# Performance work log

Hardware: AMD Instinct MI355X
Metric: run time of the kernel (lower is better)

## Reference

```python
import jax, jax.numpy as jnp
import numpy as np

B, N, D = 2, 4096, 512   # batch, tokens (64x64 latent), query_dim
H, DH = 8, 64            # heads, dim_head; inner_dim = H*DH = 512


def setup_inputs() -> dict:
    key = jax.random.key(0)
    ks = jax.random.split(key, 6)
    s = lambda fan_in: 1.0 / np.sqrt(fan_in)
    x = jax.random.normal(ks[0], (B, N, D), dtype=jnp.float32)
    Wq = jax.random.uniform(ks[1], (D, H * DH), jnp.float32, -s(D), s(D))
    Wk = jax.random.uniform(ks[2], (D, H * DH), jnp.float32, -s(D), s(D))
    Wv = jax.random.uniform(ks[3], (D, H * DH), jnp.float32, -s(D), s(D))
    Wo = jax.random.uniform(ks[4], (H * DH, D), jnp.float32, -s(H * DH), s(H * DH))
    bo = jax.random.uniform(ks[5], (D,), jnp.float32, -s(H * DH), s(H * DH))
    return {"x": x, "Wq": Wq, "Wk": Wk, "Wv": Wv, "Wo": Wo, "bo": bo}


def reference(x, Wq, Wk, Wv, Wo, bo):
    # Self-attention (context = x). Projections (no bias).
    q = x @ Wq  # [B, N, H*DH]
    k = x @ Wk
    v = x @ Wv
    split = lambda t: t.reshape(B, N, H, DH).transpose(0, 2, 1, 3)  # [B, H, N, DH]
    q, k, v = split(q), split(k), split(v)
    scale = DH ** -0.5
    # fp32 upcast for scores (ATTN_PRECISION == 'fp32' path)
    sim = jnp.einsum('bhid,bhjd->bhij', q.astype(jnp.float32), k.astype(jnp.float32)) * scale
    attn = jax.nn.softmax(sim, axis=-1).astype(v.dtype)
    out = jnp.einsum('bhij,bhjd->bhid', attn, v)           # [B, H, N, DH]
    out = out.transpose(0, 2, 1, 3).reshape(B, N, H * DH)  # [B, N, H*DH]
    return out @ Wo + bo  # to_out Linear (dropout=0)
```

## Files before the change

### kernel.cpp

```cpp
#include <hip/hip_runtime.h>
#include <hip/hip_bf16.h>
#include <stdint.h>


typedef short short8 __attribute__((ext_vector_type(8)));
typedef float f32x4 __attribute__((ext_vector_type(4)));
typedef float f32x16 __attribute__((ext_vector_type(16)));

#define QK_SCALE 0.18033688011112042f

static __device__ __forceinline__ unsigned short f32_to_bf16(float f) {
    union { float f; uint32_t u; } v; v.f = f;
    uint32_t u = v.u;
    u += 0x7FFFu + ((u >> 16) & 1u);
    return (unsigned short)(u >> 16);
}

static __device__ __forceinline__ uint32_t cvt_pk_bf16(float lo, float hi) {
    uint32_t r;
    asm("v_cvt_pk_bf16_f32 %0, %1, %2" : "=v"(r) : "v"(lo), "v"(hi));
    return r;
}

static __device__ __forceinline__ int swz(int row, int byte_in_row) {
    return row * 128 + (byte_in_row ^ ((row & 7) << 4));
}

static __device__ __forceinline__ void gload16(const void* g, void* l) {
    __builtin_amdgcn_global_load_lds(
        (const __attribute__((address_space(1))) unsigned int*)g,
        (__attribute__((address_space(3))) unsigned int*)l, 16, 0, 0);
}

union PAU { uint32_t d[4]; short8 v; };

__global__ __launch_bounds__(256) void convert_weights(
    const float* __restrict__ Wq, const float* __restrict__ Wk,
    const float* __restrict__ Wv, const float* __restrict__ Wo,
    unsigned short* __restrict__ wt)
{
    __shared__ float lds[64][65];
    const int mat = blockIdx.z;
    const float* W = (mat == 0) ? Wq : (mat == 1) ? Wk : (mat == 2) ? Wv : Wo;
    const float scale = (mat == 0) ? QK_SCALE : 1.0f;
    unsigned short* out = wt + (size_t)mat * 512 * 512;
    const int k0 = blockIdx.y * 64, n0 = blockIdx.x * 64;
    for (int i = 0; i < 16; i++) {
        int idx = threadIdx.x + i * 256;
        int kl = idx >> 6, nl = idx & 63;
        lds[kl][nl] = W[(size_t)(k0 + kl) * 512 + n0 + nl];
    }
    __syncthreads();
    for (int i = 0; i < 16; i++) {
        int idx = threadIdx.x + i * 256;
        int nr = idx >> 6, kc = idx & 63;
        out[(size_t)(n0 + nr) * 512 + k0 + kc] = f32_to_bf16(lds[kc][nr] * scale);
    }
}

__global__ __launch_bounds__(256) void convert_x(
    const float* __restrict__ x, unsigned short* __restrict__ xbf)
{
    const int idx = (blockIdx.x * 256 + threadIdx.x) * 8;
    float4 f0 = *reinterpret_cast<const float4*>(x + idx);
    float4 f1 = *reinterpret_cast<const float4*>(x + idx + 4);
    short8 v;
    v[0] = (short)f32_to_bf16(f0.x); v[1] = (short)f32_to_bf16(f0.y);
    v[2] = (short)f32_to_bf16(f0.z); v[3] = (short)f32_to_bf16(f0.w);
    v[4] = (short)f32_to_bf16(f1.x); v[5] = (short)f32_to_bf16(f1.y);
    v[6] = (short)f32_to_bf16(f1.z); v[7] = (short)f32_to_bf16(f1.w);
    *reinterpret_cast<short8*>(xbf + idx) = v;
}

__global__ __launch_bounds__(256, 2) void proj_gemm(
    const unsigned short* __restrict__ xbf,
    const unsigned short* __restrict__ wt,
    unsigned short* __restrict__ q_ws,
    unsigned short* __restrict__ k_ws,
    unsigned short* __restrict__ vt_ws)
{
    __shared__ __attribute__((aligned(16))) char smem[65536];
    const int which = blockIdx.z;
    const unsigned short* W = wt + (size_t)which * 512 * 512;
    const int m0 = blockIdx.y * 128, n0 = blockIdx.x * 128;
    const int tid = threadIdx.x, lane = tid & 63, wid = tid >> 6;
    const int wm = (wid >> 1) * 64, wn = (wid & 1) * 64;
    const int rsub = lane >> 3;
    const int cb = ((lane & 7) ^ rsub) << 4;

    f32x4 acc[4][4];
#pragma unroll
    for (int i = 0; i < 4; i++)
#pragma unroll
        for (int j = 0; j < 4; j++) acc[i][j] = (f32x4){0.f, 0.f, 0.f, 0.f};

#define PSTAGE(KT, BUF)                                                           \
    {                                                                             \
        const int kk0_ = (KT) * 64;                                               \
        _Pragma("unroll")                                                         \
        for (int cj = 0; cj < 4; cj++) {                                          \
            const int chunk = wid * 4 + cj;                                       \
            const int row = chunk * 8 + rsub;                                     \
            gload16((const char*)xbf + ((size_t)(m0 + row) * 512 + kk0_) * 2 + cb,\
                    smem + (BUF) * 32768 + chunk * 1024);                         \
            gload16((const char*)W + ((size_t)(n0 + row) * 512 + kk0_) * 2 + cb,  \
                    smem + (BUF) * 32768 + 16384 + chunk * 1024);                 \
        }                                                                         \
    }

    PSTAGE(0, 0);
    __syncthreads();

    for (int kt = 0; kt < 8; kt++) {
        const int cur = kt & 1;
        if (kt + 1 < 8) PSTAGE(kt + 1, cur ^ 1);
        unsigned short* ldsA = (unsigned short*)(smem + cur * 32768);
        unsigned short* ldsB = ldsA + 8192;
#pragma unroll
        for (int ks = 0; ks < 2; ks++) {
            const int kb = ks * 64 + (lane >> 4) * 16;
            short8 a[4], b[4];
#pragma unroll
            for (int m = 0; m < 4; m++)
                a[m] = *reinterpret_cast<short8*>(ldsA + (swz(wm + m * 16 + (lane & 15), kb) >> 1));
#pragma unroll
            for (int n = 0; n < 4; n++)
                b[n] = *reinterpret_cast<short8*>(ldsB + (swz(wn + n * 16 + (lane & 15), kb) >> 1));
            __builtin_amdgcn_s_setprio(1);
#pragma unroll
            for (int m = 0; m < 4; m++)
#pragma unroll
                for (int n = 0; n < 4; n++)
                    acc[m][n] = __builtin_amdgcn_mfma_f32_16x16x32_bf16(a[m], b[n], acc[m][n], 0, 0, 0);
            __builtin_amdgcn_s_setprio(0);
        }
        __syncthreads();
    }
#pragma unroll
    for (int m = 0; m < 4; m++)
#pragma unroll
        for (int n = 0; n < 4; n++)
#pragma unroll
            for (int r = 0; r < 4; r++) {
                int mr = m0 + wm + m * 16 + (lane >> 4) * 4 + r;
                int nc = n0 + wn + n * 16 + (lane & 15);
                unsigned short hv = f32_to_bf16(acc[m][n][r]);
                int b = mr >> 12, tok = mr & 4095;
                int h = nc >> 6, d = nc & 63;
                size_t bh = (size_t)(b * 8 + h);
                if (which == 2) {
                    vt_ws[(bh * 64 + d) * 4096 + tok] = hv;
                } else {
                    unsigned short* dst = (which == 0) ? q_ws : k_ws;
                    dst[(bh * 4096 + tok) * 64 + d] = hv;
                }
            }
}

static __device__ __forceinline__ void pack_pa(const f32x16* p, short8* pa)
{
#pragma unroll
    for (int tt = 0; tt < 2; tt++) {
        uint32_t w0 = cvt_pk_bf16(p[tt][0],  p[tt][1]);
        uint32_t w1 = cvt_pk_bf16(p[tt][2],  p[tt][3]);
        uint32_t w2 = cvt_pk_bf16(p[tt][4],  p[tt][5]);
        uint32_t w3 = cvt_pk_bf16(p[tt][6],  p[tt][7]);
        uint32_t w4 = cvt_pk_bf16(p[tt][8],  p[tt][9]);
        uint32_t w5 = cvt_pk_bf16(p[tt][10], p[tt][11]);
        uint32_t w6 = cvt_pk_bf16(p[tt][12], p[tt][13]);
        uint32_t w7 = cvt_pk_bf16(p[tt][14], p[tt][15]);
        auto r02 = __builtin_amdgcn_permlane32_swap(w0, w2, false, false);
        auto r13 = __builtin_amdgcn_permlane32_swap(w1, w3, false, false);
        auto r46 = __builtin_amdgcn_permlane32_swap(w4, w6, false, false);
        auto r57 = __builtin_amdgcn_permlane32_swap(w5, w7, false, false);
        PAU ua, ub;
        ua.d[0] = r02[0]; ua.d[1] = r13[0]; ua.d[2] = r02[1]; ua.d[3] = r13[1];
        ub.d[0] = r46[0]; ub.d[1] = r57[0]; ub.d[2] = r46[1]; ub.d[3] = r57[1];
        pa[2 * tt]     = ua.v;
        pa[2 * tt + 1] = ub.v;
    }
}

static __device__ __forceinline__ void merge_store(
    f32x16 a0, f32x16 a1, float l_part, int eoff,
    char* smem, int q0, int sw, int g, int lane, int bh,
    unsigned short* __restrict__ o_ws)
{
    const int lo = lane & 31, hi = lane >> 5;
    float* accbuf = (float*)smem;
    float* lbuf   = (float*)(smem + 32768);
    __syncthreads();
    if (g == 0) {
        float* ab = accbuf + sw * 2048;
#pragma unroll
        for (int r = 0; r < 16; r++) {
            int d0 = (r & 3) + 8 * (r >> 2) + 4 * hi;
            ab[d0 * 32 + lo] = a0[r];
            ab[(d0 + 32) * 32 + lo] = a1[r];
        }
        if (hi == 0) lbuf[sw * 32 + lo] = l_part;
    }
    __syncthreads();
    if (g == 1) {
        float rl = __builtin_amdgcn_rcpf(lbuf[sw * 32 + lo] + l_part);
        const float* ab = accbuf + sw * 2048;
        char* eb = smem + 33792 + sw * 4096;
#pragma unroll
        for (int r = 0; r < 16; r++) {
            int d0 = (r & 3) + 8 * (r >> 2) + 4 * hi;
            float o0 = (ab[d0 * 32 + lo] + a0[r]) * rl;
            float o1 = (ab[(d0 + 32) * 32 + lo] + a1[r]) * rl;
            *(unsigned short*)(eb + swz(lo, d0 * 2)) = f32_to_bf16(o0);
            *(unsigned short*)(eb + swz(lo, (d0 + 32) * 2)) = f32_to_bf16(o1);
        }
        const int b = bh >> 3, h = bh & 7;
#pragma unroll
        for (int j = 0; j < 4; j++) {
            int c = lane + 64 * j;
            int row = c >> 3, cc = c & 7;
            short8 v = *reinterpret_cast<short8*>(eb + swz(row, cc * 16));
            int tok = q0 + sw * 64 + eoff + row;
            *reinterpret_cast<short8*>(o_ws + ((size_t)(b * 4096 + tok)) * 512 + h * 64 + cc * 8) = v;
        }
    }
}

__global__ __launch_bounds__(512, 2) void attn_kernel(
    const unsigned short* __restrict__ q_ws,
    const unsigned short* __restrict__ k_ws,
    const unsigned short* __restrict__ vt_ws,
    unsigned short* __restrict__ o_ws)
{
    __shared__ __attribute__((aligned(16))) char smem[65536];
    const int blk = blockIdx.x;
    const int bh = (blk & 7) * 2 + (blk >> 7);
    const int q0 = ((blk >> 3) & 15) * 256;
    const int tid = threadIdx.x, lane = tid & 63, wid = tid >> 6;
    const int g = wid >> 2, sw = wid & 3;
    const int lo = lane & 31, hi = lane >> 5;
    const unsigned short* Qb = q_ws + (size_t)bh * 4096 * 64;
    const unsigned short* Kb = k_ws + (size_t)bh * 4096 * 64 + (size_t)g * 2048 * 64;
    const unsigned short* Vb = vt_ws + (size_t)bh * 64 * 4096 + g * 2048;

    char* gbase = smem + g * 32768;

    short8 qfA[4], qfB[4];
    const int qrA = q0 + sw * 64 + lo;
#pragma unroll
    for (int s = 0; s < 4; s++) {
        qfA[s] = *reinterpret_cast<const short8*>(Qb + (size_t)qrA * 64 + s * 16 + hi * 8);
        qfB[s] = *reinterpret_cast<const short8*>(Qb + (size_t)(qrA + 32) * 64 + s * 16 + hi * 8);
    }

    short8 onesf;
    {
        unsigned short ov = (lo == 0) ? (unsigned short)0x3F80 : (unsigned short)0;
#pragma unroll
        for (int i = 0; i < 8; i++) onesf[i] = (short)ov;
    }

    f32x16 zv;
#pragma unroll
    for (int i = 0; i < 16; i++) zv[i] = 0.f;
    f32x16 accA[2], accB[2], sumA, sumB;
    accA[0] = zv; accA[1] = zv; accB[0] = zv; accB[1] = zv;
    sumA = zv; sumB = zv;

    const int rsub = lane >> 3;
    const int cb = ((lane & 7) ^ rsub) << 4;

#define STAGE(TT, BUF)                                                          \
    {                                                                           \
        const int kv0_ = (TT) * 64;                                             \
        _Pragma("unroll")                                                       \
        for (int j = 0; j < 2; j++) {                                           \
            const int chunk = sw * 2 + j;                                       \
            const int row0 = chunk * 8;                                         \
            gload16((const char*)Kb + (size_t)(kv0_ + row0 + rsub) * 128 + cb,  \
                    gbase + (BUF) * 16384 + chunk * 1024);                      \
            gload16((const char*)Vb + (size_t)(row0 + rsub) * 8192 +            \
                        (size_t)kv0_ * 2 + cb,                                  \
                    gbase + (BUF) * 16384 + 8192 + chunk * 1024);               \
        }                                                                       \
    }

    STAGE(0, 0);
    __syncthreads();

    for (int t = 0; t < 32; t++) {
        const int cur = t & 1;
        if (t + 1 < 32) STAGE(t + 1, cur ^ 1);
        unsigned short* ldsK = (unsigned short*)(gbase + cur * 16384);
        unsigned short* ldsV = ldsK + 4096;

        f32x16 pA[2], pB[2];
        pA[0] = zv; pA[1] = zv; pB[0] = zv; pB[1] = zv;
        __builtin_amdgcn_s_setprio(1);
#pragma unroll
        for (int tt = 0; tt < 2; tt++)
#pragma unroll
            for (int s = 0; s < 4; s++) {
                short8 kf = *reinterpret_cast<short8*>(&ldsK[swz(tt * 32 + lo, s * 32 + hi * 16) >> 1]);
                pA[tt] = __builtin_amdgcn_mfma_f32_32x32x16_bf16(kf, qfA[s], pA[tt], 0, 0, 0);
                pB[tt] = __builtin_amdgcn_mfma_f32_32x32x16_bf16(kf, qfB[s], pB[tt], 0, 0, 0);
            }
        __builtin_amdgcn_s_setprio(0);

#pragma unroll
        for (int tt = 0; tt < 2; tt++)
#pragma unroll
            for (int i = 0; i < 16; i++) {
                pA[tt][i] = __builtin_amdgcn_exp2f(pA[tt][i]);
                pB[tt][i] = __builtin_amdgcn_exp2f(pB[tt][i]);
            }

        short8 paA[4], paB[4];
        pack_pa(pA, paA);
        pack_pa(pB, paB);

        __builtin_amdgcn_s_setprio(1);
#pragma unroll
        for (int dt = 0; dt < 2; dt++)
#pragma unroll
            for (int s = 0; s < 4; s++) {
                short8 vf = *reinterpret_cast<short8*>(&ldsV[swz(dt * 32 + lo, s * 32 + hi * 16) >> 1]);
                accA[dt] = __builtin_amdgcn_mfma_f32_32x32x16_bf16(vf, paA[s], accA[dt], 0, 0, 0);
                accB[dt] = __builtin_amdgcn_mfma_f32_32x32x16_bf16(vf, paB[s], accB[dt], 0, 0, 0);
            }
#pragma unroll
        for (int s = 0; s < 4; s++) {
            sumA = __builtin_amdgcn_mfma_f32_32x32x16_bf16(onesf, paA[s], sumA, 0, 0, 0);
            sumB = __builtin_amdgcn_mfma_f32_32x32x16_bf16(onesf, paB[s], sumB, 0, 0, 0);
        }
        __builtin_amdgcn_s_setprio(0);

        __syncthreads();
    }

    float lA = sumA[0] + __shfl_xor(sumA[0], 32, 64);
    float lB = sumB[0] + __shfl_xor(sumB[0], 32, 64);

    merge_store(accA[0], accA[1], lA, 0,  smem, q0, sw, g, lane, bh, o_ws);
    merge_store(accB[0], accB[1], lB, 32, smem, q0, sw, g, lane, bh, o_ws);
}

__global__ __launch_bounds__(256, 2) void out_gemm(
    const unsigned short* __restrict__ o_ws,
    const unsigned short* __restrict__ wot,
    const float* __restrict__ bo,
    float* __restrict__ out)
{
    __shared__ __attribute__((aligned(16))) char smem[65536];
    const int m0 = blockIdx.y * 128, n0 = blockIdx.x * 128;
    const int tid = threadIdx.x, lane = tid & 63, wid = tid >> 6;
    const int wm = (wid >> 1) * 64, wn = (wid & 1) * 64;
    const int rsub = lane >> 3;
    const int cb = ((lane & 7) ^ rsub) << 4;

    f32x4 acc[4][4];
#pragma unroll
    for (int i = 0; i < 4; i++)
#pragma unroll
        for (int j = 0; j < 4; j++) acc[i][j] = (f32x4){0.f, 0.f, 0.f, 0.f};

#define OSTAGE(KT, BUF)                                                            \
    {                                                                              \
        const int kk0_ = (KT) * 64;                                                \
        _Pragma("unroll")                                                          \
        for (int cj = 0; cj < 4; cj++) {                                           \
            const int chunk = wid * 4 + cj;                                        \
            const int row = chunk * 8 + rsub;                                      \
            gload16((const char*)o_ws + ((size_t)(m0 + row) * 512 + kk0_) * 2 + cb,\
                    smem + (BUF) * 32768 + chunk * 1024);                          \
            gload16((const char*)wot + ((size_t)(n0 + row) * 512 + kk0_) * 2 + cb, \
                    smem + (BUF) * 32768 + 16384 + chunk * 1024);                  \
        }                                                                          \
    }

    OSTAGE(0, 0);
    __syncthreads();

    for (int kt = 0; kt < 8; kt++) {
        const int cur = kt & 1;
        if (kt + 1 < 8) OSTAGE(kt + 1, cur ^ 1);
        unsigned short* ldsA = (unsigned short*)(smem + cur * 32768);
        unsigned short* ldsB = ldsA + 8192;
#pragma unroll
        for (int ks = 0; ks < 2; ks++) {
            const int kb = ks * 64 + (lane >> 4) * 16;
            short8 a[4], b[4];
#pragma unroll
            for (int m = 0; m < 4; m++)
                a[m] = *reinterpret_cast<short8*>(ldsA + (swz(wm + m * 16 + (lane & 15), kb) >> 1));
#pragma unroll
            for (int n = 0; n < 4; n++)
                b[n] = *reinterpret_cast<short8*>(ldsB + (swz(wn + n * 16 + (lane & 15), kb) >> 1));
            __builtin_amdgcn_s_setprio(1);
#pragma unroll
            for (int m = 0; m < 4; m++)
#pragma unroll
                for (int n = 0; n < 4; n++)
                    acc[m][n] = __builtin_amdgcn_mfma_f32_16x16x32_bf16(a[m], b[n], acc[m][n], 0, 0, 0);
            __builtin_amdgcn_s_setprio(0);
        }
        __syncthreads();
    }
#pragma unroll
    for (int n = 0; n < 4; n++) {
        const int nc = n0 + wn + n * 16 + (lane & 15);
        const float bias = bo[nc];
#pragma unroll
        for (int m = 0; m < 4; m++)
#pragma unroll
            for (int r = 0; r < 4; r++) {
                int mr = m0 + wm + m * 16 + (lane >> 4) * 4 + r;
                out[(size_t)mr * 512 + nc] = acc[m][n][r] + bias;
            }
    }
}

extern "C" void kernel_launch(void* const* d_in, const int* in_sizes, int n_in,
                              void* d_out, int out_size, void* d_ws, size_t ws_size,
                              hipStream_t stream)
{
    const float* x  = (const float*)d_in[0];
    const float* Wq = (const float*)d_in[1];
    const float* Wk = (const float*)d_in[2];
    const float* Wv = (const float*)d_in[3];
    const float* Wo = (const float*)d_in[4];
    const float* bo = (const float*)d_in[5];
    float* out = (float*)d_out;

    char* ws = (char*)d_ws;
    unsigned short* wt    = (unsigned short*)(ws);
    unsigned short* q_ws  = (unsigned short*)(ws + (size_t)(2)  * 1024 * 1024);
    unsigned short* k_ws  = (unsigned short*)(ws + (size_t)(10) * 1024 * 1024);
    unsigned short* vt_ws = (unsigned short*)(ws + (size_t)(18) * 1024 * 1024);
    unsigned short* xbf   = (unsigned short*)(ws + (size_t)(26) * 1024 * 1024);
    unsigned short* o_ws  = xbf;

    convert_weights<<<dim3(8, 8, 4), 256, 0, stream>>>(Wq, Wk, Wv, Wo, wt);
    convert_x<<<dim3(2048), 256, 0, stream>>>(x, xbf);
    proj_gemm<<<dim3(4, 64, 3), 256, 0, stream>>>(xbf, wt, q_ws, k_ws, vt_ws);
    attn_kernel<<<dim3(256), 512, 0, stream>>>(q_ws, k_ws, vt_ws, o_ws);
    out_gemm<<<dim3(4, 64), 256, 0, stream>>>(o_ws, wt + (size_t)3 * 512 * 512, bo, out);
}
```

Measured before the change: 125.2 us.

## Halve attention query tile per block to double grid size and occupancy

Each attention block now covers 128 query rows instead of 256, so each wave handles a single 32-row query tile instead of two, and the grid doubles to 512 blocks. Launch bounds are raised to request four blocks per multiprocessor, and the block-to-(head, query) mapping is recomputed. The goal is more parallelism and fewer registers per wave, but every block still streams the full K/V for its head, so K/V traffic per query doubles and each K/V LDS fragment is reused by half as many MFMAs. With 64KB of shared memory per block, the requested occupancy of four blocks may not be achievable.

```diff
diff --git a/kernel.cpp b/kernel.cpp
--- a/kernel.cpp
+++ b/kernel.cpp
@@ -182,7 +182,7 @@
 }
 
 static __device__ __forceinline__ void merge_store(
-    f32x16 a0, f32x16 a1, float l_part, int eoff,
+    f32x16 a0, f32x16 a1, float l_part,
     char* smem, int q0, int sw, int g, int lane, int bh,
     unsigned short* __restrict__ o_ws)
 {
@@ -219,13 +219,13 @@
             int c = lane + 64 * j;
             int row = c >> 3, cc = c & 7;
             short8 v = *reinterpret_cast<short8*>(eb + swz(row, cc * 16));
-            int tok = q0 + sw * 64 + eoff + row;
+            int tok = q0 + sw * 32 + row;
             *reinterpret_cast<short8*>(o_ws + ((size_t)(b * 4096 + tok)) * 512 + h * 64 + cc * 8) = v;
         }
     }
 }
 
-__global__ __launch_bounds__(512, 2) void attn_kernel(
+__global__ __launch_bounds__(512, 4) void attn_kernel(
     const unsigned short* __restrict__ q_ws,
     const unsigned short* __restrict__ k_ws,
     const unsigned short* __restrict__ vt_ws,
@@ -233,8 +233,9 @@
 {
     __shared__ __attribute__((aligned(16))) char smem[65536];
     const int blk = blockIdx.x;
-    const int bh = (blk & 7) * 2 + (blk >> 7);
-    const int q0 = ((blk >> 3) & 15) * 256;
+    const int logical = (blk & 7) * 64 + (blk >> 3);
+    const int bh = logical >> 5;
+    const int q0 = (logical & 31) * 128;
     const int tid = threadIdx.x, lane = tid & 63, wid = tid >> 6;
     const int g = wid >> 2, sw = wid & 3;
     const int lo = lane & 31, hi = lane >> 5;
@@ -244,13 +245,11 @@
 
     char* gbase = smem + g * 32768;
 
-    short8 qfA[4], qfB[4];
-    const int qrA = q0 + sw * 64 + lo;
-#pragma unroll
-    for (int s = 0; s < 4; s++) {
-        qfA[s] = *reinterpret_cast<const short8*>(Qb + (size_t)qrA * 64 + s * 16 + hi * 8);
-        qfB[s] = *reinterpret_cast<const short8*>(Qb + (size_t)(qrA + 32) * 64 + s * 16 + hi * 8);
-    }
+    short8 qf[4];
+    const int qrow = q0 + sw * 32 + lo;
+#pragma unroll
+    for (int s = 0; s < 4; s++)
+        qf[s] = *reinterpret_cast<const short8*>(Qb + (size_t)qrow * 64 + s * 16 + hi * 8);
 
     short8 onesf;
     {
@@ -262,9 +261,8 @@
     f32x16 zv;
 #pragma unroll
     for (int i = 0; i < 16; i++) zv[i] = 0.f;
-    f32x16 accA[2], accB[2], sumA, sumB;
-    accA[0] = zv; accA[1] = zv; accB[0] = zv; accB[1] = zv;
-    sumA = zv; sumB = zv;
+    f32x16 acc[2], sum;
+    acc[0] = zv; acc[1] = zv; sum = zv;
 
     const int rsub = lane >> 3;
     const int cb = ((lane & 7) ^ rsub) << 4;
@@ -293,30 +291,26 @@
         unsigned short* ldsK = (unsigned short*)(gbase + cur * 16384);
         unsigned short* ldsV = ldsK + 4096;
 
-        f32x16 pA[2], pB[2];
-        pA[0] = zv; pA[1] = zv; pB[0] = zv; pB[1] = zv;
+        f32x16 p[2];
+        p[0] = zv; p[1] = zv;
         __builtin_amdgcn_s_setprio(1);
 #pragma unroll
         for (int tt = 0; tt < 2; tt++)
 #pragma unroll
             for (int s = 0; s < 4; s++) {
                 short8 kf = *reinterpret_cast<short8*>(&ldsK[swz(tt * 32 + lo, s * 32 + hi * 16) >> 1]);
-                pA[tt] = __builtin_amdgcn_mfma_f32_32x32x16_bf16(kf, qfA[s], pA[tt], 0, 0, 0);
-                pB[tt] = __builtin_amdgcn_mfma_f32_32x32x16_bf16(kf, qfB[s], pB[tt], 0, 0, 0);
+                p[tt] = __builtin_amdgcn_mfma_f32_32x32x16_bf16(kf, qf[s], p[tt], 0, 0, 0);
             }
         __builtin_amdgcn_s_setprio(0);
 
 #pragma unroll
         for (int tt = 0; tt < 2; tt++)
 #pragma unroll
-            for (int i = 0; i < 16; i++) {
-                pA[tt][i] = __builtin_amdgcn_exp2f(pA[tt][i]);
-                pB[tt][i] = __builtin_amdgcn_exp2f(pB[tt][i]);
-            }
-
-        short8 paA[4], paB[4];
-        pack_pa(pA, paA);
-        pack_pa(pB, paB);
+            for (int i = 0; i < 16; i++)
+                p[tt][i] = __builtin_amdgcn_exp2f(p[tt][i]);
+
+        short8 pa[4];
+        pack_pa(p, pa);
 
         __builtin_amdgcn_s_setprio(1);
 #pragma unroll
@@ -324,24 +318,19 @@
 #pragma unroll
             for (int s = 0; s < 4; s++) {
                 short8 vf = *reinterpret_cast<short8*>(&ldsV[swz(dt * 32 + lo, s * 32 + hi * 16) >> 1]);
-                accA[dt] = __builtin_amdgcn_mfma_f32_32x32x16_bf16(vf, paA[s], accA[dt], 0, 0, 0);
-                accB[dt] = __builtin_amdgcn_mfma_f32_32x32x16_bf16(vf, paB[s], accB[dt], 0, 0, 0);
+                acc[dt] = __builtin_amdgcn_mfma_f32_32x32x16_bf16(vf, pa[s], acc[dt], 0, 0, 0);
             }
 #pragma unroll
-        for (int s = 0; s < 4; s++) {
-            sumA = __builtin_amdgcn_mfma_f32_32x32x16_bf16(onesf, paA[s], sumA, 0, 0, 0);
-            sumB = __builtin_amdgcn_mfma_f32_32x32x16_bf16(onesf, paB[s], sumB, 0, 0, 0);
-        }
+        for (int s = 0; s < 4; s++)
+            sum = __builtin_amdgcn_mfma_f32_32x32x16_bf16(onesf, pa[s], sum, 0, 0, 0);
         __builtin_amdgcn_s_setprio(0);
 
         __syncthreads();
     }
 
-    float lA = sumA[0] + __shfl_xor(sumA[0], 32, 64);
-    float lB = sumB[0] + __shfl_xor(sumB[0], 32, 64);
-
-    merge_store(accA[0], accA[1], lA, 0,  smem, q0, sw, g, lane, bh, o_ws);
-    merge_store(accB[0], accB[1], lB, 32, smem, q0, sw, g, lane, bh, o_ws);
+    float l_part = sum[0] + __shfl_xor(sum[0], 32, 64);
+
+    merge_store(acc[0], acc[1], l_part, smem, q0, sw, g, lane, bh, o_ws);
 }
 
 __global__ __launch_bounds__(256, 2) void out_gemm(
@@ -442,6 +431,6 @@
     convert_weights<<<dim3(8, 8, 4), 256, 0, stream>>>(Wq, Wk, Wv, Wo, wt);
     convert_x<<<dim3(2048), 256, 0, stream>>>(x, xbf);
     proj_gemm<<<dim3(4, 64, 3), 256, 0, stream>>>(xbf, wt, q_ws, k_ws, vt_ws);
-    attn_kernel<<<dim3(256), 512, 0, stream>>>(q_ws, k_ws, vt_ws, o_ws);
+    attn_kernel<<<dim3(512), 512, 0, stream>>>(q_ws, k_ws, vt_ws, o_ws);
     out_gemm<<<dim3(4, 64), 256, 0, stream>>>(o_ws, wt + (size_t)3 * 512 * 512, bo, out);
 }
```

Measured after the change: 131.9 us. 5.3% more time.

## Software-pipeline attention loop: overlap PV of previous tile with exp of current

Applied to the files above, without the earlier changes.

The attention main loop is restructured so the P·V MFMAs for tile t-1 run after the QK^T MFMAs for tile t and before its exp2/pack. The single double buffer becomes a 3-deep K ring and a 4-deep V ring, with prefetch two tiles ahead and explicit vmcnt waits plus raw barriers in place of __syncthreads. The goal is to hide exp/transcendental latency behind matrix work and to deepen global-load latency hiding. LDS per block grows from 64KB to 112KB, which likely limits occupancy to one block per CU and conflicts with the launch bound of 2.

```diff
diff --git a/kernel.cpp b/kernel.cpp
--- a/kernel.cpp
+++ b/kernel.cpp
@@ -231,7 +231,7 @@
     const unsigned short* __restrict__ vt_ws,
     unsigned short* __restrict__ o_ws)
 {
-    __shared__ __attribute__((aligned(16))) char smem[65536];
+    __shared__ __attribute__((aligned(16))) char smem[114688];
     const int blk = blockIdx.x;
     const int bh = (blk & 7) * 2 + (blk >> 7);
     const int q0 = ((blk >> 3) & 15) * 256;
@@ -242,7 +242,7 @@
     const unsigned short* Kb = k_ws + (size_t)bh * 4096 * 64 + (size_t)g * 2048 * 64;
     const unsigned short* Vb = vt_ws + (size_t)bh * 64 * 4096 + g * 2048;
 
-    char* gbase = smem + g * 32768;
+    char* gbase = smem + g * 57344;
 
     short8 qfA[4], qfB[4];
     const int qrA = q0 + sw * 64 + lo;
@@ -265,33 +265,35 @@
     f32x16 accA[2], accB[2], sumA, sumB;
     accA[0] = zv; accA[1] = zv; accB[0] = zv; accB[1] = zv;
     sumA = zv; sumB = zv;
+    short8 paA[4], paB[4];
 
     const int rsub = lane >> 3;
     const int cb = ((lane & 7) ^ rsub) << 4;
 
-#define STAGE(TT, BUF)                                                          \
+#define STAGE(TT)                                                               \
     {                                                                           \
         const int kv0_ = (TT) * 64;                                             \
+        char* kdst = gbase + ((TT) % 3) * 8192;                                 \
+        char* vdst = gbase + 24576 + ((TT) % 4) * 8192;                         \
         _Pragma("unroll")                                                       \
         for (int j = 0; j < 2; j++) {                                           \
             const int chunk = sw * 2 + j;                                       \
             const int row0 = chunk * 8;                                         \
             gload16((const char*)Kb + (size_t)(kv0_ + row0 + rsub) * 128 + cb,  \
-                    gbase + (BUF) * 16384 + chunk * 1024);                      \
+                    kdst + chunk * 1024);                                       \
             gload16((const char*)Vb + (size_t)(row0 + rsub) * 8192 +            \
                         (size_t)kv0_ * 2 + cb,                                  \
-                    gbase + (BUF) * 16384 + 8192 + chunk * 1024);               \
+                    vdst + chunk * 1024);                                       \
         }                                                                       \
     }
 
-    STAGE(0, 0);
-    __syncthreads();
+    STAGE(0);
+    STAGE(1);
+    asm volatile("s_waitcnt vmcnt(4)" ::: "memory");
+    __builtin_amdgcn_s_barrier();
 
     for (int t = 0; t < 32; t++) {
-        const int cur = t & 1;
-        if (t + 1 < 32) STAGE(t + 1, cur ^ 1);
-        unsigned short* ldsK = (unsigned short*)(gbase + cur * 16384);
-        unsigned short* ldsV = ldsK + 4096;
+        unsigned short* ldsK = (unsigned short*)(gbase + (t % 3) * 8192);
 
         f32x16 pA[2], pB[2];
         pA[0] = zv; pA[1] = zv; pB[0] = zv; pB[1] = zv;
@@ -306,6 +308,27 @@
             }
         __builtin_amdgcn_s_setprio(0);
 
+        if (t < 30) STAGE(t + 2);
+
+        if (t > 0) {
+            unsigned short* ldsVp = (unsigned short*)(gbase + 24576 + ((t - 1) % 4) * 8192);
+            __builtin_amdgcn_s_setprio(1);
+#pragma unroll
+            for (int dt = 0; dt < 2; dt++)
+#pragma unroll
+                for (int s = 0; s < 4; s++) {
+                    short8 vf = *reinterpret_cast<short8*>(&ldsVp[swz(dt * 32 + lo, s * 32 + hi * 16) >> 1]);
+                    accA[dt] = __builtin_amdgcn_mfma_f32_32x32x16_bf16(vf, paA[s], accA[dt], 0, 0, 0);
+                    accB[dt] = __builtin_amdgcn_mfma_f32_32x32x16_bf16(vf, paB[s], accB[dt], 0, 0, 0);
+                }
+#pragma unroll
+            for (int s = 0; s < 4; s++) {
+                sumA = __builtin_amdgcn_mfma_f32_32x32x16_bf16(onesf, paA[s], sumA, 0, 0, 0);
+                sumB = __builtin_amdgcn_mfma_f32_32x32x16_bf16(onesf, paB[s], sumB, 0, 0, 0);
+            }
+            __builtin_amdgcn_s_setprio(0);
+        }
+
 #pragma unroll
         for (int tt = 0; tt < 2; tt++)
 #pragma unroll
@@ -313,17 +336,25 @@
                 pA[tt][i] = __builtin_amdgcn_exp2f(pA[tt][i]);
                 pB[tt][i] = __builtin_amdgcn_exp2f(pB[tt][i]);
             }
-
-        short8 paA[4], paB[4];
         pack_pa(pA, paA);
         pack_pa(pB, paB);
 
-        __builtin_amdgcn_s_setprio(1);
+        if (t < 30) {
+            asm volatile("s_waitcnt vmcnt(4) lgkmcnt(0)" ::: "memory");
+            __builtin_amdgcn_s_barrier();
+        } else if (t == 30) {
+            asm volatile("s_waitcnt vmcnt(0) lgkmcnt(0)" ::: "memory");
+            __builtin_amdgcn_s_barrier();
+        }
+    }
+
+    {
+        unsigned short* ldsVp = (unsigned short*)(gbase + 24576 + (31 % 4) * 8192);
 #pragma unroll
         for (int dt = 0; dt < 2; dt++)
 #pragma unroll
             for (int s = 0; s < 4; s++) {
-                short8 vf = *reinterpret_cast<short8*>(&ldsV[swz(dt * 32 + lo, s * 32 + hi * 16) >> 1]);
+                short8 vf = *reinterpret_cast<short8*>(&ldsVp[swz(dt * 32 + lo, s * 32 + hi * 16) >> 1]);
                 accA[dt] = __builtin_amdgcn_mfma_f32_32x32x16_bf16(vf, paA[s], accA[dt], 0, 0, 0);
                 accB[dt] = __builtin_amdgcn_mfma_f32_32x32x16_bf16(vf, paB[s], accB[dt], 0, 0, 0);
             }
@@ -332,9 +363,6 @@
             sumA = __builtin_amdgcn_mfma_f32_32x32x16_bf16(onesf, paA[s], sumA, 0, 0, 0);
             sumB = __builtin_amdgcn_mfma_f32_32x32x16_bf16(onesf, paB[s], sumB, 0, 0, 0);
         }
-        __builtin_amdgcn_s_setprio(0);
-
-        __syncthreads();
     }
 
     float lA = sumA[0] + __shfl_xor(sumA[0], 32, 64);
```

Measured after the change: 130.7 us (median of 2 runs). +4.4%, slower.

## Load K/V fragments directly to registers and fuse conversion kernels

Applied to the files above, without the earlier changes.

The attention kernel drops its LDS double-buffered staging of K and V and its barriers. Instead it loads MFMA fragments straight from global memory into registers, ping-ponging two K register sets and loading V after the QK matmul. The row-sum MFMAs against a ones vector are replaced with scalar accumulation of the exp values. The weight and x conversion kernels are merged into one launch to save a kernel launch. Register pressure rises, and global loads now have no cooperative reuse across waves, so more L2 traffic is possible.

```diff
diff --git a/kernel.cpp b/kernel.cpp
--- a/kernel.cpp
+++ b/kernel.cpp
@@ -34,42 +34,42 @@
 
 union PAU { uint32_t d[4]; short8 v; };
 
-__global__ __launch_bounds__(256) void convert_weights(
+__global__ __launch_bounds__(256) void convert_pre(
+    const float* __restrict__ x,
     const float* __restrict__ Wq, const float* __restrict__ Wk,
     const float* __restrict__ Wv, const float* __restrict__ Wo,
-    unsigned short* __restrict__ wt)
+    unsigned short* __restrict__ wt, unsigned short* __restrict__ xbf)
 {
     __shared__ float lds[64][65];
-    const int mat = blockIdx.z;
-    const float* W = (mat == 0) ? Wq : (mat == 1) ? Wk : (mat == 2) ? Wv : Wo;
-    const float scale = (mat == 0) ? QK_SCALE : 1.0f;
-    unsigned short* out = wt + (size_t)mat * 512 * 512;
-    const int k0 = blockIdx.y * 64, n0 = blockIdx.x * 64;
-    for (int i = 0; i < 16; i++) {
-        int idx = threadIdx.x + i * 256;
-        int kl = idx >> 6, nl = idx & 63;
-        lds[kl][nl] = W[(size_t)(k0 + kl) * 512 + n0 + nl];
-    }
-    __syncthreads();
-    for (int i = 0; i < 16; i++) {
-        int idx = threadIdx.x + i * 256;
-        int nr = idx >> 6, kc = idx & 63;
-        out[(size_t)(n0 + nr) * 512 + k0 + kc] = f32_to_bf16(lds[kc][nr] * scale);
-    }
-}
-
-__global__ __launch_bounds__(256) void convert_x(
-    const float* __restrict__ x, unsigned short* __restrict__ xbf)
-{
-    const int idx = (blockIdx.x * 256 + threadIdx.x) * 8;
-    float4 f0 = *reinterpret_cast<const float4*>(x + idx);
-    float4 f1 = *reinterpret_cast<const float4*>(x + idx + 4);
-    short8 v;
-    v[0] = (short)f32_to_bf16(f0.x); v[1] = (short)f32_to_bf16(f0.y);
-    v[2] = (short)f32_to_bf16(f0.z); v[3] = (short)f32_to_bf16(f0.w);
-    v[4] = (short)f32_to_bf16(f1.x); v[5] = (short)f32_to_bf16(f1.y);
-    v[6] = (short)f32_to_bf16(f1.z); v[7] = (short)f32_to_bf16(f1.w);
-    *reinterpret_cast<short8*>(xbf + idx) = v;
+    const int bx = blockIdx.x;
+    if (bx < 256) {
+        const int mat = bx >> 6, rem = bx & 63;
+        const int k0 = (rem >> 3) * 64, n0 = (rem & 7) * 64;
+        const float* W = (mat == 0) ? Wq : (mat == 1) ? Wk : (mat == 2) ? Wv : Wo;
+        const float scale = (mat == 0) ? QK_SCALE : 1.0f;
+        unsigned short* out = wt + (size_t)mat * 512 * 512;
+        for (int i = 0; i < 16; i++) {
+            int idx = threadIdx.x + i * 256;
+            int kl = idx >> 6, nl = idx & 63;
+            lds[kl][nl] = W[(size_t)(k0 + kl) * 512 + n0 + nl];
+        }
+        __syncthreads();
+        for (int i = 0; i < 16; i++) {
+            int idx = threadIdx.x + i * 256;
+            int nr = idx >> 6, kc = idx & 63;
+            out[(size_t)(n0 + nr) * 512 + k0 + kc] = f32_to_bf16(lds[kc][nr] * scale);
+        }
+    } else {
+        const int idx = ((bx - 256) * 256 + threadIdx.x) * 8;
+        float4 f0 = *reinterpret_cast<const float4*>(x + idx);
+        float4 f1 = *reinterpret_cast<const float4*>(x + idx + 4);
+        short8 v;
+        v[0] = (short)f32_to_bf16(f0.x); v[1] = (short)f32_to_bf16(f0.y);
+        v[2] = (short)f32_to_bf16(f0.z); v[3] = (short)f32_to_bf16(f0.w);
+        v[4] = (short)f32_to_bf16(f1.x); v[5] = (short)f32_to_bf16(f1.y);
+        v[6] = (short)f32_to_bf16(f1.z); v[7] = (short)f32_to_bf16(f1.w);
+        *reinterpret_cast<short8*>(xbf + idx) = v;
+    }
 }
 
 __global__ __launch_bounds__(256, 2) void proj_gemm(
@@ -231,7 +231,7 @@
     const unsigned short* __restrict__ vt_ws,
     unsigned short* __restrict__ o_ws)
 {
-    __shared__ __attribute__((aligned(16))) char smem[65536];
+    __shared__ __attribute__((aligned(16))) char smem[50176];
     const int blk = blockIdx.x;
     const int bh = (blk & 7) * 2 + (blk >> 7);
     const int q0 = ((blk >> 3) & 15) * 256;
@@ -242,8 +242,6 @@
     const unsigned short* Kb = k_ws + (size_t)bh * 4096 * 64 + (size_t)g * 2048 * 64;
     const unsigned short* Vb = vt_ws + (size_t)bh * 64 * 4096 + g * 2048;
 
-    char* gbase = smem + g * 32768;
-
     short8 qfA[4], qfB[4];
     const int qrA = q0 + sw * 64 + lo;
 #pragma unroll
@@ -252,93 +250,77 @@
         qfB[s] = *reinterpret_cast<const short8*>(Qb + (size_t)(qrA + 32) * 64 + s * 16 + hi * 8);
     }
 
-    short8 onesf;
-    {
-        unsigned short ov = (lo == 0) ? (unsigned short)0x3F80 : (unsigned short)0;
-#pragma unroll
-        for (int i = 0; i < 8; i++) onesf[i] = (short)ov;
-    }
-
     f32x16 zv;
 #pragma unroll
     for (int i = 0; i < 16; i++) zv[i] = 0.f;
-    f32x16 accA[2], accB[2], sumA, sumB;
+    f32x16 accA[2], accB[2];
     accA[0] = zv; accA[1] = zv; accB[0] = zv; accB[1] = zv;
-    sumA = zv; sumB = zv;
-
-    const int rsub = lane >> 3;
-    const int cb = ((lane & 7) ^ rsub) << 4;
-
-#define STAGE(TT, BUF)                                                          \
-    {                                                                           \
-        const int kv0_ = (TT) * 64;                                             \
-        _Pragma("unroll")                                                       \
-        for (int j = 0; j < 2; j++) {                                           \
-            const int chunk = sw * 2 + j;                                       \
-            const int row0 = chunk * 8;                                         \
-            gload16((const char*)Kb + (size_t)(kv0_ + row0 + rsub) * 128 + cb,  \
-                    gbase + (BUF) * 16384 + chunk * 1024);                      \
-            gload16((const char*)Vb + (size_t)(row0 + rsub) * 8192 +            \
-                        (size_t)kv0_ * 2 + cb,                                  \
-                    gbase + (BUF) * 16384 + 8192 + chunk * 1024);               \
-        }                                                                       \
-    }
-
-    STAGE(0, 0);
-    __syncthreads();
-
-    for (int t = 0; t < 32; t++) {
-        const int cur = t & 1;
-        if (t + 1 < 32) STAGE(t + 1, cur ^ 1);
-        unsigned short* ldsK = (unsigned short*)(gbase + cur * 16384);
-        unsigned short* ldsV = ldsK + 4096;
-
-        f32x16 pA[2], pB[2];
-        pA[0] = zv; pA[1] = zv; pB[0] = zv; pB[1] = zv;
-        __builtin_amdgcn_s_setprio(1);
-#pragma unroll
-        for (int tt = 0; tt < 2; tt++)
-#pragma unroll
-            for (int s = 0; s < 4; s++) {
-                short8 kf = *reinterpret_cast<short8*>(&ldsK[swz(tt * 32 + lo, s * 32 + hi * 16) >> 1]);
-                pA[tt] = __builtin_amdgcn_mfma_f32_32x32x16_bf16(kf, qfA[s], pA[tt], 0, 0, 0);
-                pB[tt] = __builtin_amdgcn_mfma_f32_32x32x16_bf16(kf, qfB[s], pB[tt], 0, 0, 0);
-            }
-        __builtin_amdgcn_s_setprio(0);
-
-#pragma unroll
-        for (int tt = 0; tt < 2; tt++)
-#pragma unroll
-            for (int i = 0; i < 16; i++) {
-                pA[tt][i] = __builtin_amdgcn_exp2f(pA[tt][i]);
-                pB[tt][i] = __builtin_amdgcn_exp2f(pB[tt][i]);
-            }
-
-        short8 paA[4], paB[4];
-        pack_pa(pA, paA);
-        pack_pa(pB, paB);
-
-        __builtin_amdgcn_s_setprio(1);
-#pragma unroll
-        for (int dt = 0; dt < 2; dt++)
-#pragma unroll
-            for (int s = 0; s < 4; s++) {
-                short8 vf = *reinterpret_cast<short8*>(&ldsV[swz(dt * 32 + lo, s * 32 + hi * 16) >> 1]);
-                accA[dt] = __builtin_amdgcn_mfma_f32_32x32x16_bf16(vf, paA[s], accA[dt], 0, 0, 0);
-                accB[dt] = __builtin_amdgcn_mfma_f32_32x32x16_bf16(vf, paB[s], accB[dt], 0, 0, 0);
-            }
-#pragma unroll
-        for (int s = 0; s < 4; s++) {
-            sumA = __builtin_amdgcn_mfma_f32_32x32x16_bf16(onesf, paA[s], sumA, 0, 0, 0);
-            sumB = __builtin_amdgcn_mfma_f32_32x32x16_bf16(onesf, paB[s], sumB, 0, 0, 0);
-        }
-        __builtin_amdgcn_s_setprio(0);
-
-        __syncthreads();
-    }
-
-    float lA = sumA[0] + __shfl_xor(sumA[0], 32, 64);
-    float lB = sumB[0] + __shfl_xor(sumB[0], 32, 64);
+    float lsA0 = 0.f, lsA1 = 0.f, lsA2 = 0.f, lsA3 = 0.f;
+    float lsB0 = 0.f, lsB1 = 0.f, lsB2 = 0.f, lsB3 = 0.f;
+
+    short8 k0[2][4], k1[2][4], vr[2][4];
+
+#define LOADK(T, KR) { const size_t kvo_ = (size_t)(T) * 64;                     \
+    _Pragma("unroll") for (int tt = 0; tt < 2; tt++)                             \
+    _Pragma("unroll") for (int s = 0; s < 4; s++)                                \
+        KR[tt][s] = *reinterpret_cast<const short8*>(                            \
+            Kb + (kvo_ + tt * 32 + lo) * 64 + s * 16 + hi * 8); }
+
+#define LOADV(T) { const size_t kvo_ = (size_t)(T) * 64;                         \
+    _Pragma("unroll") for (int dt = 0; dt < 2; dt++)                             \
+    _Pragma("unroll") for (int s = 0; s < 4; s++)                                \
+        vr[dt][s] = *reinterpret_cast<const short8*>(                            \
+            Vb + (size_t)(dt * 32 + lo) * 4096 + kvo_ + s * 16 + hi * 8); }
+
+#define ABODY(T, KR) {                                                           \
+    f32x16 pA[2], pB[2];                                                         \
+    pA[0] = zv; pA[1] = zv; pB[0] = zv; pB[1] = zv;                              \
+    __builtin_amdgcn_s_setprio(1);                                               \
+    _Pragma("unroll") for (int tt = 0; tt < 2; tt++)                             \
+    _Pragma("unroll") for (int s = 0; s < 4; s++) {                              \
+        pA[tt] = __builtin_amdgcn_mfma_f32_32x32x16_bf16(KR[tt][s], qfA[s], pA[tt], 0, 0, 0); \
+        pB[tt] = __builtin_amdgcn_mfma_f32_32x32x16_bf16(KR[tt][s], qfB[s], pB[tt], 0, 0, 0); \
+    }                                                                            \
+    __builtin_amdgcn_s_setprio(0);                                               \
+    LOADV(T);                                                                    \
+    _Pragma("unroll") for (int tt = 0; tt < 2; tt++)                             \
+    _Pragma("unroll") for (int i = 0; i < 16; i += 4) {                          \
+        float a0 = __builtin_amdgcn_exp2f(pA[tt][i]);                            \
+        float a1 = __builtin_amdgcn_exp2f(pA[tt][i + 1]);                        \
+        float a2 = __builtin_amdgcn_exp2f(pA[tt][i + 2]);                        \
+        float a3 = __builtin_amdgcn_exp2f(pA[tt][i + 3]);                        \
+        float b0 = __builtin_amdgcn_exp2f(pB[tt][i]);                            \
+        float b1 = __builtin_amdgcn_exp2f(pB[tt][i + 1]);                        \
+        float b2 = __builtin_amdgcn_exp2f(pB[tt][i + 2]);                        \
+        float b3 = __builtin_amdgcn_exp2f(pB[tt][i + 3]);                        \
+        pA[tt][i] = a0; pA[tt][i + 1] = a1; pA[tt][i + 2] = a2; pA[tt][i + 3] = a3; \
+        pB[tt][i] = b0; pB[tt][i + 1] = b1; pB[tt][i + 2] = b2; pB[tt][i + 3] = b3; \
+        lsA0 += a0; lsA1 += a1; lsA2 += a2; lsA3 += a3;                          \
+        lsB0 += b0; lsB1 += b1; lsB2 += b2; lsB3 += b3;                          \
+    }                                                                            \
+    short8 paA[4], paB[4];                                                       \
+    pack_pa(pA, paA); pack_pa(pB, paB);                                          \
+    __builtin_amdgcn_s_setprio(1);                                               \
+    _Pragma("unroll") for (int dt = 0; dt < 2; dt++)                             \
+    _Pragma("unroll") for (int s = 0; s < 4; s++) {                              \
+        accA[dt] = __builtin_amdgcn_mfma_f32_32x32x16_bf16(vr[dt][s], paA[s], accA[dt], 0, 0, 0); \
+        accB[dt] = __builtin_amdgcn_mfma_f32_32x32x16_bf16(vr[dt][s], paB[s], accB[dt], 0, 0, 0); \
+    }                                                                            \
+    __builtin_amdgcn_s_setprio(0); }
+
+    LOADK(0, k0);
+#pragma unroll 1
+    for (int j = 0; j < 16; j++) {
+        LOADK(2 * j + 1, k1);
+        ABODY(2 * j, k0);
+        if (j < 15) LOADK(2 * j + 2, k0);
+        ABODY(2 * j + 1, k1);
+    }
+
+    float lA = (lsA0 + lsA1) + (lsA2 + lsA3);
+    float lB = (lsB0 + lsB1) + (lsB2 + lsB3);
+    lA += __shfl_xor(lA, 32, 64);
+    lB += __shfl_xor(lB, 32, 64);
 
     merge_store(accA[0], accA[1], lA, 0,  smem, q0, sw, g, lane, bh, o_ws);
     merge_store(accB[0], accB[1], lB, 32, smem, q0, sw, g, lane, bh, o_ws);
@@ -439,8 +421,7 @@
     unsigned short* xbf   = (unsigned short*)(ws + (size_t)(26) * 1024 * 1024);
     unsigned short* o_ws  = xbf;
 
-    convert_weights<<<dim3(8, 8, 4), 256, 0, stream>>>(Wq, Wk, Wv, Wo, wt);
-    convert_x<<<dim3(2048), 256, 0, stream>>>(x, xbf);
+    convert_pre<<<dim3(2304), 256, 0, stream>>>(x, Wq, Wk, Wv, Wo, wt, xbf);
     proj_gemm<<<dim3(4, 64, 3), 256, 0, stream>>>(xbf, wt, q_ws, k_ws, vt_ws);
     attn_kernel<<<dim3(256), 512, 0, stream>>>(q_ws, k_ws, vt_ws, o_ws);
     out_gemm<<<dim3(4, 64), 256, 0, stream>>>(o_ws, wt + (size_t)3 * 512 * 512, bo, out);
```

After: 251.0 us. 2x slower.
